# Kernel optimization log

Hardware: AMD Instinct MI355X
Metric: run time of the kernel (lower is better)

## Reference

```python
import jax, jax.numpy as jnp
import numpy as np

S_STATES, C_TYPES, G_GENES = 16, 64, 20000


def setup_inputs() -> dict:
    key = jax.random.key(0)
    k1, k2, k3, k4 = jax.random.split(key, 4)
    Z_mu = jax.random.normal(k1, (C_TYPES, G_GENES), dtype=jnp.float32)
    # positive log-normal sigmas, moderate scale for numerical stability
    Z_sigma = jax.random.uniform(k2, (C_TYPES, G_GENES), dtype=jnp.float32) * 0.5 + 0.1
    # build a valid correlation matrix (PSD with unit diagonal) so var >= 0
    L = jax.random.normal(k3, (C_TYPES, C_TYPES), dtype=jnp.float32)
    cov = L @ L.T + C_TYPES * jnp.eye(C_TYPES, dtype=jnp.float32)
    d = jnp.sqrt(jnp.diag(cov))
    corr = cov / (d[:, None] * d[None, :])
    # cell_prob rows on the simplex (Dirichlet-like), per state
    cell_prob = jax.nn.softmax(jax.random.normal(k4, (S_STATES, C_TYPES), dtype=jnp.float32), axis=1)
    return {"Z_mu": Z_mu, "Z_sigma": Z_sigma, "corr": corr, "cell_prob": cell_prob}


def reference(Z_mu, Z_sigma, corr, cell_prob):
    """Vectorized LogNorm.calculate_mu_sigma.

    Z_mu, Z_sigma: (C, G); corr: (C, C); cell_prob: (S, C).
    Returns mu, sigma of shape (S, G) -- moment-matched log-normal sum params
    for every (state, gene) pair, matching the nested-loop torch original.
    """
    # EV[s,c,g] = exp(mu + sigma^2/2) * w  (first moment of each component, weighted)
    ev_base = jnp.exp(Z_mu + 0.5 * Z_sigma ** 2)            # (C, G)
    EV = cell_prob[:, :, None] * ev_base[None, :, :]         # (S, C, G)
    Ssum = EV.sum(axis=1)                                    # (S, G)
    # A[s,c,g] = EV * sigma; var = sum_{c,d} A_c corr_{cd} A_d / Ssum^2
    A = EV * Z_sigma[None, :, :]                             # (S, C, G)
    var = jnp.einsum('scg,cd,sdg->sg', A, corr, A) / (Ssum ** 2)  # (S, G)
    mu_s = jnp.log(Ssum) - 0.5 * var
    sigma_s = jnp.sqrt(var)
    return (mu_s, sigma_s)
```

## Files before the change

kernel.cpp:

```cpp
#include <hip/hip_runtime.h>
#include <hip/hip_bf16.h>


#define S_STATES 16
#define C_TYPES  64
#define G_GENES  20000
#define OUT_HALF (S_STATES * G_GENES)
#define NPAIR    96
#define PER_WAVE 24

typedef __attribute__((ext_vector_type(8))) short bf16x8;
typedef __attribute__((ext_vector_type(4))) float f32x4;

static __device__ __forceinline__ short f2bf(float f) {
    union { __hip_bfloat16 h; short s; } u;
    u.h = __float2bfloat16(f);
    return u.s;
}

__global__ __launch_bounds__(64)
void build_A(const float* __restrict__ corr, const float* __restrict__ w,
             short* __restrict__ cwA)
{
    const int p    = blockIdx.x;
    const int lane = threadIdx.x;
    const int gl   = lane & 15;
    const int q    = lane >> 4;
    bf16x8 v;
    if (p < NPAIR) {
        const int dh = (p >= 64);
        const int c  = dh ? p - 32 : p;
        const int d0 = dh * 32 + q * 8;
        const float wc = w[gl * C_TYPES + c];
#pragma unroll
        for (int j = 0; j < 8; ++j) {
            const int d = d0 + j;
            const float sc = (d < c) ? 2.0f : (d == c ? 1.0f : 0.0f);
            v[j] = f2bf(sc * corr[c * C_TYPES + d] * wc * w[gl * C_TYPES + d]);
        }
    } else {
        const int k0 = (p - NPAIR) * 32 + q * 8;
#pragma unroll
        for (int j = 0; j < 8; ++j)
            v[j] = f2bf(w[gl * C_TYPES + k0 + j]);
    }
    *(bf16x8*)(cwA + (p << 9) + lane * 8) = v;
}

__global__ __launch_bounds__(256, 3)
void lognorm_main(const float* __restrict__ Z_mu,
                  const float* __restrict__ Z_sigma,
                  const short* __restrict__ cwA,
                  float* __restrict__ out)
{
    __shared__ float x1s[C_TYPES][33];
    __shared__ float x2s[C_TYPES][33];
    __shared__ float accs[4][S_STATES][33];
    __shared__ float ssum_s[S_STATES][33];

    const int gt    = blockIdx.x;
    const int tid   = threadIdx.x;
    const int w     = tid >> 6;
    const int lane  = tid & 63;
    const int gl    = lane & 15;
    const int q     = lane >> 4;
    const int gbase = gt * 32;

    {
        const int d  = tid >> 2;
        const int g0 = (tid & 3) * 4;
        const float* zm = Z_mu    + d * G_GENES + gbase + g0;
        const float* zs = Z_sigma + d * G_GENES + gbase + g0;
        const float4 m0 = *(const float4*)zm, m1 = *(const float4*)(zm + 16);
        const float4 s0 = *(const float4*)zs, s1 = *(const float4*)(zs + 16);
        float e;
        e = __expf(fmaf(0.5f*s0.x, s0.x, m0.x)); x1s[d][g0+0]    = e; x2s[d][g0+0]    = e*s0.x;
        e = __expf(fmaf(0.5f*s0.y, s0.y, m0.y)); x1s[d][g0+1]    = e; x2s[d][g0+1]    = e*s0.y;
        e = __expf(fmaf(0.5f*s0.z, s0.z, m0.z)); x1s[d][g0+2]    = e; x2s[d][g0+2]    = e*s0.z;
        e = __expf(fmaf(0.5f*s0.w, s0.w, m0.w)); x1s[d][g0+3]    = e; x2s[d][g0+3]    = e*s0.w;
        e = __expf(fmaf(0.5f*s1.x, s1.x, m1.x)); x1s[d][g0+16]   = e; x2s[d][g0+16]   = e*s1.x;
        e = __expf(fmaf(0.5f*s1.y, s1.y, m1.y)); x1s[d][g0+17]   = e; x2s[d][g0+17]   = e*s1.y;
        e = __expf(fmaf(0.5f*s1.z, s1.z, m1.z)); x1s[d][g0+18]   = e; x2s[d][g0+18]   = e*s1.z;
        e = __expf(fmaf(0.5f*s1.w, s1.w, m1.w)); x1s[d][g0+19]   = e; x2s[d][g0+19]   = e*s1.w;
    }
    __syncthreads();

    float xc[PER_WAVE][2];
#pragma unroll
    for (int i = 0; i < PER_WAVE; ++i) {
        const int p = i * 4 + w;
        const int c = (i >= 16) ? p - 32 : p;
#pragma unroll
        for (int t = 0; t < 2; ++t) xc[i][t] = x2s[c][gl + t * 16];
    }
    float xh[2][8][2];
#pragma unroll
    for (int dh = 0; dh < 2; ++dh)
#pragma unroll
        for (int j = 0; j < 8; ++j)
#pragma unroll
            for (int t = 0; t < 2; ++t)
                xh[dh][j][t] = x2s[dh * 32 + q * 8 + j][gl + t * 16];

    const short* Abase = cwA + (w << 9) + lane * 8;
    f32x4 acc0 = {0.f, 0.f, 0.f, 0.f}, acc1 = {0.f, 0.f, 0.f, 0.f};
#pragma unroll
    for (int i = 0; i < PER_WAVE; ++i) {
        const bf16x8 af = *(const bf16x8*)(Abase + (i << 11));
        const int dh = (i >= 16) ? 1 : 0;
        bf16x8 b0, b1;
#pragma unroll
        for (int j = 0; j < 8; ++j) {
            b0[j] = f2bf(xc[i][0] * xh[dh][j][0]);
            b1[j] = f2bf(xc[i][1] * xh[dh][j][1]);
        }
        acc0 = __builtin_amdgcn_mfma_f32_16x16x32_bf16(af, b0, acc0, 0, 0, 0);
        acc1 = __builtin_amdgcn_mfma_f32_16x16x32_bf16(af, b1, acc1, 0, 0, 0);
    }
#pragma unroll
    for (int r = 0; r < 4; ++r) {
        accs[w][q * 4 + r][gl]      = acc0[r];
        accs[w][q * 4 + r][gl + 16] = acc1[r];
    }

    if (w < 2) {
        bf16x8 x1f[2], wf[2];
#pragma unroll
        for (int kk = 0; kk < 2; ++kk) {
            wf[kk] = *(const bf16x8*)(cwA + ((NPAIR + kk) << 9) + lane * 8);
#pragma unroll
            for (int j = 0; j < 8; ++j)
                x1f[kk][j] = f2bf(x1s[kk * 32 + q * 8 + j][gl + w * 16]);
        }
        f32x4 sa = {0.f, 0.f, 0.f, 0.f};
        sa = __builtin_amdgcn_mfma_f32_16x16x32_bf16(wf[0], x1f[0], sa, 0, 0, 0);
        sa = __builtin_amdgcn_mfma_f32_16x16x32_bf16(wf[1], x1f[1], sa, 0, 0, 0);
#pragma unroll
        for (int r = 0; r < 4; ++r) ssum_s[q * 4 + r][gl + w * 16] = sa[r];
    }
    __syncthreads();

    const int s  = tid >> 4;
    const int gx = tid & 15;
#pragma unroll
    for (int t = 0; t < 2; ++t) {
        const int gg = gx + t * 16;
        const float vn = (accs[0][s][gg] + accs[1][s][gg])
                       + (accs[2][s][gg] + accs[3][s][gg]);
        const float ss   = ssum_s[s][gg];
        const float rvar = fmaxf(vn, 0.f) / (ss * ss);
        out[s * G_GENES + gbase + gg]            = __logf(ss) - 0.5f * rvar;
        out[OUT_HALF + s * G_GENES + gbase + gg] = sqrtf(rvar);
    }
}

extern "C" void kernel_launch(void* const* d_in, const int* in_sizes, int n_in,
                              void* d_out, int out_size, void* d_ws, size_t ws_size,
                              hipStream_t stream) {
    const float* Z_mu      = (const float*)d_in[0];
    const float* Z_sigma   = (const float*)d_in[1];
    const float* corr      = (const float*)d_in[2];
    const float* cell_prob = (const float*)d_in[3];
    float* out = (float*)d_out;
    short* cwA = (short*)d_ws;

    build_A<<<dim3(NPAIR + 2), dim3(64), 0, stream>>>(corr, cell_prob, cwA);

    const int gtiles = G_GENES / 32;
    lognorm_main<<<dim3(gtiles), dim3(256), 0, stream>>>(
        Z_mu, Z_sigma, cwA, out);
}
```

Before: 17.29 us.

## Switch MFMA operands from bf16 to fp16 with packed products and transposed LDS

Converts the MFMA path from bf16 to fp16, so B fragments are built with packed half2 multiplies instead of per-element float multiply plus bf16 conversion. The exponentials are pre-scaled by 0.25 to keep values within fp16 range, and the log output is corrected by adding ln(4). Shared memory is reorganised into packed half2, transposed layouts so fragment loads become wider, and build_A uses float4 loads. This reduces VALU and conversion work in the inner loop, at the cost of fp16 overflow or precision risk if the inputs grow larger.

```diff
diff --git a/kernel.cpp b/kernel.cpp
--- a/kernel.cpp
+++ b/kernel.cpp
@@ -1,5 +1,4 @@
 #include <hip/hip_runtime.h>
-#include <hip/hip_bf16.h>
 
 
 #define S_STATES 16
@@ -9,52 +8,58 @@
 #define NPAIR    96
 #define PER_WAVE 24
 
-typedef __attribute__((ext_vector_type(8))) short bf16x8;
-typedef __attribute__((ext_vector_type(4))) float f32x4;
-
-static __device__ __forceinline__ short f2bf(float f) {
-    union { __hip_bfloat16 h; short s; } u;
-    u.h = __float2bfloat16(f);
-    return u.s;
-}
+typedef _Float16 f16x2 __attribute__((ext_vector_type(2)));
+typedef _Float16 f16x8 __attribute__((ext_vector_type(8)));
+typedef float    f32x4 __attribute__((ext_vector_type(4)));
+
+union Frag8 { f16x2 p[4]; f16x8 v; uint4 u; _Float16 h[8]; };
 
 __global__ __launch_bounds__(64)
 void build_A(const float* __restrict__ corr, const float* __restrict__ w,
-             short* __restrict__ cwA)
+             unsigned short* __restrict__ cwA)
 {
     const int p    = blockIdx.x;
     const int lane = threadIdx.x;
     const int gl   = lane & 15;
     const int q    = lane >> 4;
-    bf16x8 v;
+    Frag8 v;
     if (p < NPAIR) {
         const int dh = (p >= 64);
         const int c  = dh ? p - 32 : p;
         const int d0 = dh * 32 + q * 8;
         const float wc = w[gl * C_TYPES + c];
+        const float4 c0 = *(const float4*)(corr + c * C_TYPES + d0);
+        const float4 c1 = *(const float4*)(corr + c * C_TYPES + d0 + 4);
+        const float4 w0 = *(const float4*)(w + gl * C_TYPES + d0);
+        const float4 w1 = *(const float4*)(w + gl * C_TYPES + d0 + 4);
+        const float cv[8] = {c0.x,c0.y,c0.z,c0.w,c1.x,c1.y,c1.z,c1.w};
+        const float wv[8] = {w0.x,w0.y,w0.z,w0.w,w1.x,w1.y,w1.z,w1.w};
 #pragma unroll
         for (int j = 0; j < 8; ++j) {
             const int d = d0 + j;
             const float sc = (d < c) ? 2.0f : (d == c ? 1.0f : 0.0f);
-            v[j] = f2bf(sc * corr[c * C_TYPES + d] * wc * w[gl * C_TYPES + d]);
+            v.h[j] = (_Float16)(sc * cv[j] * wc * wv[j]);
         }
     } else {
         const int k0 = (p - NPAIR) * 32 + q * 8;
-#pragma unroll
-        for (int j = 0; j < 8; ++j)
-            v[j] = f2bf(w[gl * C_TYPES + k0 + j]);
-    }
-    *(bf16x8*)(cwA + (p << 9) + lane * 8) = v;
+        const float4 w0 = *(const float4*)(w + gl * C_TYPES + k0);
+        const float4 w1 = *(const float4*)(w + gl * C_TYPES + k0 + 4);
+        const float wv[8] = {w0.x,w0.y,w0.z,w0.w,w1.x,w1.y,w1.z,w1.w};
+#pragma unroll
+        for (int j = 0; j < 8; ++j) v.h[j] = (_Float16)wv[j];
+    }
+    *(uint4*)(cwA + (p << 9) + lane * 8) = v.u;
 }
 
 __global__ __launch_bounds__(256, 3)
 void lognorm_main(const float* __restrict__ Z_mu,
                   const float* __restrict__ Z_sigma,
-                  const short* __restrict__ cwA,
+                  const unsigned short* __restrict__ cwA,
                   float* __restrict__ out)
 {
-    __shared__ float x1s[C_TYPES][33];
-    __shared__ float x2s[C_TYPES][33];
+    __shared__ f16x2 x2pT[32][35];
+    __shared__ f16x2 x1pT[32][35];
+    __shared__ f16x2 x2tp[C_TYPES][21];
     __shared__ float accs[4][S_STATES][33];
     __shared__ float ssum_s[S_STATES][33];
 
@@ -67,76 +72,103 @@
     const int gbase = gt * 32;
 
     {
-        const int d  = tid >> 2;
-        const int g0 = (tid & 3) * 4;
-        const float* zm = Z_mu    + d * G_GENES + gbase + g0;
-        const float* zs = Z_sigma + d * G_GENES + gbase + g0;
-        const float4 m0 = *(const float4*)zm, m1 = *(const float4*)(zm + 16);
-        const float4 s0 = *(const float4*)zs, s1 = *(const float4*)(zs + 16);
-        float e;
-        e = __expf(fmaf(0.5f*s0.x, s0.x, m0.x)); x1s[d][g0+0]    = e; x2s[d][g0+0]    = e*s0.x;
-        e = __expf(fmaf(0.5f*s0.y, s0.y, m0.y)); x1s[d][g0+1]    = e; x2s[d][g0+1]    = e*s0.y;
-        e = __expf(fmaf(0.5f*s0.z, s0.z, m0.z)); x1s[d][g0+2]    = e; x2s[d][g0+2]    = e*s0.z;
-        e = __expf(fmaf(0.5f*s0.w, s0.w, m0.w)); x1s[d][g0+3]    = e; x2s[d][g0+3]    = e*s0.w;
-        e = __expf(fmaf(0.5f*s1.x, s1.x, m1.x)); x1s[d][g0+16]   = e; x2s[d][g0+16]   = e*s1.x;
-        e = __expf(fmaf(0.5f*s1.y, s1.y, m1.y)); x1s[d][g0+17]   = e; x2s[d][g0+17]   = e*s1.y;
-        e = __expf(fmaf(0.5f*s1.z, s1.z, m1.z)); x1s[d][g0+18]   = e; x2s[d][g0+18]   = e*s1.z;
-        e = __expf(fmaf(0.5f*s1.w, s1.w, m1.w)); x1s[d][g0+19]   = e; x2s[d][g0+19]   = e*s1.w;
+        const int dp = tid >> 3;
+        const int gq = tid & 7;
+        const int ga = gq * 2;
+        const float* zm0 = Z_mu    + (2*dp) * G_GENES + gbase + ga;
+        const float* zs0 = Z_sigma + (2*dp) * G_GENES + gbase + ga;
+        const float2 m00 = *(const float2*)zm0;
+        const float2 m01 = *(const float2*)(zm0 + 16);
+        const float2 m10 = *(const float2*)(zm0 + G_GENES);
+        const float2 m11 = *(const float2*)(zm0 + G_GENES + 16);
+        const float2 s00 = *(const float2*)zs0;
+        const float2 s01 = *(const float2*)(zs0 + 16);
+        const float2 s10 = *(const float2*)(zs0 + G_GENES);
+        const float2 s11 = *(const float2*)(zs0 + G_GENES + 16);
+        float x1v[2][2][2], x2v[2][2][2];
+#define XDO(r,h,j,M,S) { const float s_=(S); const float e_=__expf(fmaf(0.5f*s_,s_,(M)))*0.25f; \
+                         x1v[r][h][j]=e_; x2v[r][h][j]=e_*s_; }
+        XDO(0,0,0, m00.x, s00.x) XDO(0,0,1, m00.y, s00.y)
+        XDO(0,1,0, m01.x, s01.x) XDO(0,1,1, m01.y, s01.y)
+        XDO(1,0,0, m10.x, s10.x) XDO(1,0,1, m10.y, s10.y)
+        XDO(1,1,0, m11.x, s11.x) XDO(1,1,1, m11.y, s11.y)
+#undef XDO
+#pragma unroll
+        for (int h = 0; h < 2; ++h)
+#pragma unroll
+            for (int j = 0; j < 2; ++j) {
+                const int g = ga + j + 16 * h;
+                f16x2 a, b;
+                a.x = (_Float16)x2v[0][h][j]; a.y = (_Float16)x2v[1][h][j];
+                b.x = (_Float16)x1v[0][h][j]; b.y = (_Float16)x1v[1][h][j];
+                x2pT[g][dp] = a;
+                x1pT[g][dp] = b;
+            }
+#pragma unroll
+        for (int r = 0; r < 2; ++r)
+#pragma unroll
+            for (int j = 0; j < 2; ++j) {
+                f16x2 a;
+                a.x = (_Float16)x2v[r][0][j];
+                a.y = (_Float16)x2v[r][1][j];
+                x2tp[2*dp + r][ga + j] = a;
+            }
     }
     __syncthreads();
 
-    float xc[PER_WAVE][2];
+    f16x2 xh[2][4][2];
+#pragma unroll
+    for (int dh = 0; dh < 2; ++dh)
+#pragma unroll
+        for (int t = 0; t < 2; ++t)
+#pragma unroll
+            for (int jp = 0; jp < 4; ++jp)
+                xh[dh][jp][t] = x2pT[gl + 16*t][dh*16 + q*4 + jp];
+
+    f16x2 xct[PER_WAVE];
 #pragma unroll
     for (int i = 0; i < PER_WAVE; ++i) {
-        const int p = i * 4 + w;
-        const int c = (i >= 16) ? p - 32 : p;
-#pragma unroll
-        for (int t = 0; t < 2; ++t) xc[i][t] = x2s[c][gl + t * 16];
-    }
-    float xh[2][8][2];
-#pragma unroll
-    for (int dh = 0; dh < 2; ++dh)
-#pragma unroll
-        for (int j = 0; j < 8; ++j)
-#pragma unroll
-            for (int t = 0; t < 2; ++t)
-                xh[dh][j][t] = x2s[dh * 32 + q * 8 + j][gl + t * 16];
-
-    const short* Abase = cwA + (w << 9) + lane * 8;
-    f32x4 acc0 = {0.f, 0.f, 0.f, 0.f}, acc1 = {0.f, 0.f, 0.f, 0.f};
+        const int c = i*4 + w - ((i >= 16) ? 32 : 0);
+        xct[i] = x2tp[c][gl];
+    }
+
+    const unsigned short* Abase = cwA + (w << 9) + lane * 8;
+    f32x4 acc0 = {0.f,0.f,0.f,0.f}, acc1 = {0.f,0.f,0.f,0.f};
 #pragma unroll
     for (int i = 0; i < PER_WAVE; ++i) {
-        const bf16x8 af = *(const bf16x8*)(Abase + (i << 11));
+        Frag8 af; af.u = *(const uint4*)(Abase + (i << 11));
         const int dh = (i >= 16) ? 1 : 0;
-        bf16x8 b0, b1;
-#pragma unroll
-        for (int j = 0; j < 8; ++j) {
-            b0[j] = f2bf(xc[i][0] * xh[dh][j][0]);
-            b1[j] = f2bf(xc[i][1] * xh[dh][j][1]);
+        Frag8 b0, b1;
+#pragma unroll
+        for (int jp = 0; jp < 4; ++jp) {
+            f16x2 s0; s0.x = xct[i].x; s0.y = xct[i].x;
+            f16x2 s1; s1.x = xct[i].y; s1.y = xct[i].y;
+            b0.p[jp] = s0 * xh[dh][jp][0];
+            b1.p[jp] = s1 * xh[dh][jp][1];
         }
-        acc0 = __builtin_amdgcn_mfma_f32_16x16x32_bf16(af, b0, acc0, 0, 0, 0);
-        acc1 = __builtin_amdgcn_mfma_f32_16x16x32_bf16(af, b1, acc1, 0, 0, 0);
+        acc0 = __builtin_amdgcn_mfma_f32_16x16x32_f16(af.v, b0.v, acc0, 0, 0, 0);
+        acc1 = __builtin_amdgcn_mfma_f32_16x16x32_f16(af.v, b1.v, acc1, 0, 0, 0);
     }
 #pragma unroll
     for (int r = 0; r < 4; ++r) {
-        accs[w][q * 4 + r][gl]      = acc0[r];
-        accs[w][q * 4 + r][gl + 16] = acc1[r];
+        accs[w][q*4 + r][gl]      = acc0[r];
+        accs[w][q*4 + r][gl + 16] = acc1[r];
     }
 
     if (w < 2) {
-        bf16x8 x1f[2], wf[2];
+        Frag8 x1f[2], wf[2];
 #pragma unroll
         for (int kk = 0; kk < 2; ++kk) {
-            wf[kk] = *(const bf16x8*)(cwA + ((NPAIR + kk) << 9) + lane * 8);
-#pragma unroll
-            for (int j = 0; j < 8; ++j)
-                x1f[kk][j] = f2bf(x1s[kk * 32 + q * 8 + j][gl + w * 16]);
+            wf[kk].u = *(const uint4*)(cwA + ((NPAIR + kk) << 9) + lane * 8);
+#pragma unroll
+            for (int jp = 0; jp < 4; ++jp)
+                x1f[kk].p[jp] = x1pT[gl + 16*w][kk*16 + q*4 + jp];
         }
-        f32x4 sa = {0.f, 0.f, 0.f, 0.f};
-        sa = __builtin_amdgcn_mfma_f32_16x16x32_bf16(wf[0], x1f[0], sa, 0, 0, 0);
-        sa = __builtin_amdgcn_mfma_f32_16x16x32_bf16(wf[1], x1f[1], sa, 0, 0, 0);
-#pragma unroll
-        for (int r = 0; r < 4; ++r) ssum_s[q * 4 + r][gl + w * 16] = sa[r];
+        f32x4 sa = {0.f,0.f,0.f,0.f};
+        sa = __builtin_amdgcn_mfma_f32_16x16x32_f16(wf[0].v, x1f[0].v, sa, 0, 0, 0);
+        sa = __builtin_amdgcn_mfma_f32_16x16x32_f16(wf[1].v, x1f[1].v, sa, 0, 0, 0);
+#pragma unroll
+        for (int r = 0; r < 4; ++r) ssum_s[q*4 + r][gl + 16*w] = sa[r];
     }
     __syncthreads();
 
@@ -144,12 +176,13 @@
     const int gx = tid & 15;
 #pragma unroll
     for (int t = 0; t < 2; ++t) {
-        const int gg = gx + t * 16;
+        const int gg = gx + 16 * t;
         const float vn = (accs[0][s][gg] + accs[1][s][gg])
                        + (accs[2][s][gg] + accs[3][s][gg]);
         const float ss   = ssum_s[s][gg];
         const float rvar = fmaxf(vn, 0.f) / (ss * ss);
-        out[s * G_GENES + gbase + gg]            = __logf(ss) - 0.5f * rvar;
+        out[s * G_GENES + gbase + gg] =
+            __logf(ss) + 1.3862943611f - 0.5f * rvar;
         out[OUT_HALF + s * G_GENES + gbase + gg] = sqrtf(rvar);
     }
 }
@@ -162,7 +195,7 @@
     const float* corr      = (const float*)d_in[2];
     const float* cell_prob = (const float*)d_in[3];
     float* out = (float*)d_out;
-    short* cwA = (short*)d_ws;
+    unsigned short* cwA = (unsigned short*)d_ws;
 
     build_A<<<dim3(NPAIR + 2), dim3(64), 0, stream>>>(corr, cell_prob, cwA);
 
```

Measured after the change: 15.41 us. -10.9%, faster.
